# Kernel optimization log

Hardware: AMD Instinct MI355X
Metric: run time of the kernel (lower is better)

Reference implementation:

```python
import jax, jax.numpy as jnp
import numpy as np

KH = KW = 3  # fixed: distortion() generates a 9-tap (3x3) offset grid


def make_offset(h, w, dilation=1.0, skydome=True):
    """Faithful numpy port of DistortionConvLayer.distortion -> [1,h,w,9,2] (last dim = [x_off, y_off])."""
    pi = np.pi
    unit_w = 2.0 * pi / w
    unit_h = pi / (2.0 * h) if skydome else pi / h
    rho = np.tan(unit_w) * dilation
    v = np.array([0.0, 1.0, 0.0])
    r_grid = np.array([[1, -1], [1, 0], [1, 1], [0, -1], [0, 0], [0, 1], [-1, -1], [-1, 0], [-1, 1]], dtype=np.float64)
    xc = int(w * 0.5)
    theta = (xc - 0.5 * w) * unit_w
    y = np.arange(h, dtype=np.float64)
    phi = (h - y) * unit_h if skydome else (h * 0.5 - y) * unit_h  # [h]
    p_u = np.stack([np.cos(phi) * np.cos(theta), np.sin(phi), np.cos(phi) * np.sin(theta)], axis=-1)  # [h,3]
    t_x = np.cross(np.broadcast_to(v, p_u.shape), p_u)  # [h,3]
    t_y = np.cross(p_u, t_x)                            # [h,3]
    # r_sphere: [h,9,3]
    r_sphere = rho * (r_grid[None, :, 0, None] * t_x[:, None, :] + r_grid[None, :, 1, None] * t_y[:, None, :])
    p_ur = p_u[:, None, :] + r_sphere  # [h,9,3]
    ux, uy, uz = p_ur[..., 0], p_ur[..., 1], p_ur[..., 2]
    base = np.arctan2(uz, ux)
    theta_r = np.where(ux > 0, base,
               np.where(ux < 0, np.where(uz >= 0, base + pi, base - pi),
                np.where(uz > 0, pi * 0.5, -pi * 0.5)))
    phi_r = np.arcsin(uy)
    x_r = (theta_r / pi + 1.0) * 0.5 * w
    y_r = (1.0 - 2.0 * phi_r / pi) * h if skydome else (0.5 - phi_r / pi) * h
    k = np.stack([x_r, y_r], axis=-1)          # [h,9,2], entries [x, y] (as in original)
    off = k - k[:, 4:5, :]                      # subtract center tap
    off = np.broadcast_to(off[:, None, :, :], (h, w, 9, 2))  # tile over width
    return off[None].astype(np.float32)         # [1,h,w,9,2]


def setup_inputs() -> dict:
    key = jax.random.key(0)
    k1, k2 = jax.random.split(key)
    B, H, W, C, F = 4, 128, 256, 64, 128
    inputs = jax.random.normal(k1, (B, H, W, C), dtype=jnp.float32)
    fan_in = KH * KW * C
    kernel = jax.random.normal(k2, (fan_in, F), dtype=jnp.float32) * (1.0 / np.sqrt(fan_in))
    bias = jnp.zeros((F,), dtype=jnp.float32)
    return {"inputs": inputs, "kernel": kernel, "bias": bias}


def reference(inputs, kernel, bias):
    B, H, W, C = inputs.shape
    F = kernel.shape[1]
    off = jnp.asarray(make_offset(H, W))  # [1,H,W,9,2], static constant
    # 'same' padding for 3x3, stride 1, dilation 1 -> pad 1 on each side
    xp = jnp.pad(inputs, ((0, 0), (1, 1), (1, 1), (0, 0)))
    in_h, in_w = H + 2, W + 2
    # base conv sampling coordinates (extract_patches order: tap k -> dy=k//3, dx=k%3)
    dy = jnp.repeat(jnp.arange(KH), KW).astype(jnp.float32)  # [9]
    dx = jnp.tile(jnp.arange(KW), KH).astype(jnp.float32)    # [9]
    base_y = jnp.arange(H, dtype=jnp.float32)[None, :, None, None] + dy[None, None, None, :]  # [1,H,1,9]
    base_x = jnp.arange(W, dtype=jnp.float32)[None, None, :, None] + dx[None, None, None, :]  # [1,1,W,9]
    # NOTE: faithful to original: channel 0 of offset (x_r diffs) is added to y, channel 1 to x
    y = base_y + off[..., 0]  # [1,H,W,9]
    x = base_x + off[..., 1]
    y = jnp.clip(y, 0.0, in_h - 1)
    x = jnp.where(x < 0, x + in_w, x)
    x = jnp.where(x > in_w - 1, x - in_w, x)
    y0 = jnp.floor(y).astype(jnp.int32)
    x0 = jnp.floor(x).astype(jnp.int32)
    y1, x1 = y0 + 1, x0 + 1
    y0 = jnp.clip(y0, 0, in_h - 1); y1 = jnp.clip(y1, 0, in_h - 1)
    x0 = jnp.clip(x0, 0, in_w - 1); x1 = jnp.clip(x1, 0, in_w - 1)
    bidx = jnp.arange(B)[:, None, None, None]  # [B,1,1,1], broadcasts against [1,H,W,9]
    gather = lambda yi, xi: xp[bidx, yi, xi]   # -> [B,H,W,9,C]
    p0 = gather(y0, x0); p1 = gather(y0, x1); p2 = gather(y1, x0); p3 = gather(y1, x1)
    y0f, y1f = y0.astype(jnp.float32), y1.astype(jnp.float32)
    x0f, x1f = x0.astype(jnp.float32), x1.astype(jnp.float32)
    w0 = ((y1f - y) * (x1f - x))[..., None]
    w1 = ((y1f - y) * (x - x0f))[..., None]
    w2 = ((y - y0f) * (x1f - x))[..., None]
    w3 = ((y - y0f) * (x - x0f))[..., None]
    pixels = w0 * p0 + w1 * p1 + w2 * p2 + w3 * p3  # [B,H,W,9,C]
    pixels = pixels.reshape(B, H * W, KH * KW * C)
    out = pixels @ kernel + bias                    # [B,HW,F]
    return jax.nn.relu(out.reshape(B, H, W, F))
```

## Files before the change

### kernel.cpp

```cpp
#include <hip/hip_runtime.h>
#include <math.h>

#define Bb 4
#define Hh 128
#define Ww 256
#define Cc 64
#define Ff 128
#define INH 130
#define INW 258

#define WSLOT 72
#define WPW 37

typedef __attribute__((ext_vector_type(8))) __bf16 bf16x8;
typedef __attribute__((ext_vector_type(4))) float floatx4;

__device__ __forceinline__ unsigned short f2bf(float f) {
  unsigned int u = __float_as_uint(f);
  unsigned int r = u + 0x7fffu + ((u >> 16) & 1u);
  return (unsigned short)(r >> 16);
}

__device__ __forceinline__ unsigned int cvt_pk_bf16(float lo, float hi) {
  unsigned int r;
  asm("v_cvt_pk_bf16_f32 %0, %1, %2" : "=v"(r) : "v"(lo), "v"(hi));
  return r;
}

__global__ void prep_kernel(const float* __restrict__ kmat,
                            float* __restrict__ offtab,
                            unsigned short* __restrict__ kTB) {
  int gid = blockIdx.x * 256 + threadIdx.x;
  if (gid < 576 * 128) {
    int f = gid & 127;
    int k = gid >> 7;
    int tap = k >> 6;
    int r = k & 63;
    int kk = r >> 5;
    int quad = (r >> 3) & 3;
    int i = r & 7;
    int chunk = tap * 8 + kk * 4 + quad;
    kTB[((size_t)chunk * 128 + f) * 8 + i] = f2bf(kmat[gid]);
  }
  if (gid < Hh * 9) {
    int h = gid / 9;
    int j = gid - h * 9;
    const double pi = 3.14159265358979323846;
    double unit_w = 2.0 * pi / (double)Ww;
    double unit_h = pi / (2.0 * (double)Hh);
    double rho = tan(unit_w);
    double theta = ((double)(Ww / 2) - 0.5 * (double)Ww) * unit_w;
    double phi = ((double)Hh - (double)h) * unit_h;
    double cph = cos(phi), sph = sin(phi);
    double cth = cos(theta), sth = sin(theta);
    double pux = cph * cth, puy = sph, puz = cph * sth;
    double txx = puz, txy = 0.0, txz = -pux;
    double tyx = puy * txz - puz * txy;
    double tyy = puz * txx - pux * txz;
    double tyz = pux * txy - puy * txx;
    const int r0t[9] = {1, 1, 1, 0, 0, 0, -1, -1, -1};
    const int r1t[9] = {-1, 0, 1, -1, 0, 1, -1, 0, 1};
    auto proj = [&](int r0, int r1, double& xr, double& yr) {
      double ux = pux + rho * ((double)r0 * txx + (double)r1 * tyx);
      double uy = puy + rho * ((double)r0 * txy + (double)r1 * tyy);
      double uz = puz + rho * ((double)r0 * txz + (double)r1 * tyz);
      double base = atan2(uz, ux);
      double th;
      if (ux > 0.0)        th = base;
      else if (ux < 0.0)   th = (uz >= 0.0) ? base + pi : base - pi;
      else                 th = (uz > 0.0) ? pi * 0.5 : -pi * 0.5;
      double ph = asin(uy);
      xr = (th / pi + 1.0) * 0.5 * (double)Ww;
      yr = (1.0 - 2.0 * ph / pi) * (double)Hh;
    };
    double xc, yc, xj, yj;
    proj(0, 0, xc, yc);
    proj(r0t[j], r1t[j], xj, yj);
    offtab[gid * 2 + 0] = (float)(xj - xc);
    offtab[gid * 2 + 1] = (float)(yj - yc);
  }
}

__global__ __launch_bounds__(256, 3) void fused_kernel(
    const float* __restrict__ in, const float* __restrict__ bias,
    const unsigned short* __restrict__ kTB, const float* __restrict__ offtab,
    float* __restrict__ out) {
  __shared__ unsigned short winH[4 * WPW * WSLOT];

  int lidx = ((blockIdx.x & 7) << 7) | (blockIdx.x >> 3);
  int wt = lidx & 1;
  int h  = (lidx >> 1) & 127;
  int b  = lidx >> 8;
  int w0 = wt << 7;

  int tid  = threadIdx.x;
  int lane = tid & 63;
  int wave = tid >> 6;
  int m_base = wave << 5;
  int l15  = lane & 15;
  int quad = lane >> 4;

  unsigned short* win = &winH[wave * (WPW * WSLOT)];
  if (lane < 18) *(uint2*)&win[36 * WSLOT + lane * 4] = (uint2){0u, 0u};

  floatx4 acc[2][8];
#pragma unroll
  for (int i = 0; i < 2; i++)
#pragma unroll
    for (int j = 0; j < 8; j++) acc[i][j] = (floatx4){0.f, 0.f, 0.f, 0.f};

  const float* inb = in + (size_t)b * Hh * Ww * Cc;
  const bf16x8* kbase = (const bf16x8*)kTB;

  for (int tap = 0; tap < 9; tap++) {
    float off0 = offtab[(h * 9 + tap) * 2 + 0];
    float off1 = offtab[(h * 9 + tap) * 2 + 1];
    float dyk = (float)(tap / 3), dxk = (float)(tap % 3);

    float y = (float)h + dyk + off0;
    y = fminf(fmaxf(y, 0.f), (float)(INH - 1));
    int y0i = (int)floorf(y);
    int y1i = y0i + 1;
    y0i = min(max(y0i, 0), INH - 1);
    y1i = min(max(y1i, 0), INH - 1);
    float wy0 = (float)y1i - y;
    float wy1 = y - (float)y0i;
    if (!(y0i >= 1 && y0i <= Hh)) wy0 = 0.f;
    if (!(y1i >= 1 && y1i <= Hh)) wy1 = 0.f;
    const char* r0 = (const char*)(inb + (size_t)min(max(y0i - 1, 0), Hh - 1) * Ww * Cc);
    const char* r1 = (const char*)(inb + (size_t)min(max(y1i - 1, 0), Hh - 1) * Ww * Cc);

    float xrep = (float)w0 + dxk + off1;
    float flo  = floorf(xrep);
    int jb = (int)flo - 1;
    float fr = xrep - flo;
    float q00 = wy0 * (1.f - fr), q01 = wy0 * fr;
    float q10 = wy1 * (1.f - fr), q11 = wy1 * fr;

    int slotv[2];
#pragma unroll
    for (int mi = 0; mi < 2; mi++) {
      int wr = m_base + mi * 16 + l15;
      float x = (float)(w0 + wr) + dxk + off1;
      if (x < 0.f) x += (float)INW;
      if (x > (float)(INW - 1)) x -= (float)INW;
      int x0i = (int)floorf(x);
      int s = x0i - jb;
      if (s < 0) s += INW;
      int ls = s - m_base;
      if ((unsigned)ls > 35u) ls = 36;
      slotv[mi] = ls;
    }

    for (int it = 0; it < 5; it++) {
      int t = lane + (it << 6);
      if (t < 36 * 8) {
        int ls = t >> 3;
        int c8 = (t & 7) << 3;
        int col = jb + m_base + ls;
        if (col < 0) col += INW;
        if (col > INW - 1) col -= INW;
        int ncol = (col == INW - 1) ? 0 : col + 1;
        bool cok = ((unsigned)(col - 1) < (unsigned)Ww);
        bool nok = ((unsigned)(ncol - 1) < (unsigned)Ww);
        unsigned offc = (((unsigned)((col - 1) & (Ww - 1))) << 8) + ((unsigned)c8 << 2);
        unsigned offn = (((unsigned)((ncol - 1) & (Ww - 1))) << 8) + ((unsigned)c8 << 2);
        float w00 = cok ? q00 : 0.f;
        float w01 = nok ? q01 : 0.f;
        float w10 = cok ? q10 : 0.f;
        float w11 = nok ? q11 : 0.f;
        uint4 st;
        {
          float4 a0 = *(const float4*)(r0 + offc);
          float4 a1 = *(const float4*)(r0 + offn);
          float4 b0 = *(const float4*)(r1 + offc);
          float4 b1 = *(const float4*)(r1 + offn);
          float px = w00 * a0.x + w01 * a1.x + w10 * b0.x + w11 * b1.x;
          float py = w00 * a0.y + w01 * a1.y + w10 * b0.y + w11 * b1.y;
          float pz = w00 * a0.z + w01 * a1.z + w10 * b0.z + w11 * b1.z;
          float pw = w00 * a0.w + w01 * a1.w + w10 * b0.w + w11 * b1.w;
          st.x = cvt_pk_bf16(px, py);
          st.y = cvt_pk_bf16(pz, pw);
        }
        {
          float4 a0 = *(const float4*)(r0 + offc + 16);
          float4 a1 = *(const float4*)(r0 + offn + 16);
          float4 b0 = *(const float4*)(r1 + offc + 16);
          float4 b1 = *(const float4*)(r1 + offn + 16);
          float px = w00 * a0.x + w01 * a1.x + w10 * b0.x + w11 * b1.x;
          float py = w00 * a0.y + w01 * a1.y + w10 * b0.y + w11 * b1.y;
          float pz = w00 * a0.z + w01 * a1.z + w10 * b0.z + w11 * b1.z;
          float pw = w00 * a0.w + w01 * a1.w + w10 * b0.w + w11 * b1.w;
          st.z = cvt_pk_bf16(px, py);
          st.w = cvt_pk_bf16(pz, pw);
        }
        *(uint4*)(&win[ls * WSLOT + c8]) = st;
      }
    }

#pragma unroll
    for (int kk = 0; kk < 2; kk++) {
      int ch0 = (tap * 8 + kk * 4 + quad) * 128;
      bf16x8 af0 = *(const bf16x8*)&win[slotv[0] * WSLOT + kk * 32 + quad * 8];
      bf16x8 af1 = *(const bf16x8*)&win[slotv[1] * WSLOT + kk * 32 + quad * 8];
#pragma unroll
      for (int ni = 0; ni < 8; ni++) {
        bf16x8 bf = kbase[ch0 + ni * 16 + l15];
        acc[0][ni] = __builtin_amdgcn_mfma_f32_16x16x32_bf16(af0, bf, acc[0][ni], 0, 0, 0);
        acc[1][ni] = __builtin_amdgcn_mfma_f32_16x16x32_bf16(af1, bf, acc[1][ni], 0, 0, 0);
      }
    }
  }

  size_t outbase = ((size_t)(b * Hh + h) * Ww + w0);
#pragma unroll
  for (int ni = 0; ni < 8; ni++) {
    int f = ni * 16 + l15;
    float bv = bias[f];
#pragma unroll
    for (int mi = 0; mi < 2; mi++) {
#pragma unroll
      for (int r = 0; r < 4; r++) {
        int m = m_base + mi * 16 + quad * 4 + r;
        out[(outbase + m) * Ff + f] = fmaxf(acc[mi][ni][r] + bv, 0.f);
      }
    }
  }
}

extern "C" void kernel_launch(void* const* d_in, const int* in_sizes, int n_in,
                              void* d_out, int out_size, void* d_ws, size_t ws_size,
                              hipStream_t stream) {
  const float* in   = (const float*)d_in[0];
  const float* kmat = (const float*)d_in[1];
  const float* bias = (const float*)d_in[2];
  float* out = (float*)d_out;

  float* offtab = (float*)d_ws;
  unsigned short* kTB = (unsigned short*)((char*)d_ws + Hh * 9 * 2 * sizeof(float));
  if (ws_size < (size_t)(Hh * 9 * 2 * sizeof(float) + 128 * 576 * sizeof(unsigned short)))
    return;

  prep_kernel<<<288, 256, 0, stream>>>(kmat, offtab, kTB);
  fused_kernel<<<Bb * Hh * (Ww / 128), 256, 0, stream>>>(in, bias, kTB, offtab, out);
}
```

Before: 156.5 us.

## Split bilinear sampling into y-interp staging and x-interp at fragment load

The staging loop now does only the vertical interpolation, loading one column instead of two (half the global loads). It stores fp32 rows in LDS. The horizontal lerp between adjacent slots and the bf16 conversion move to the point where MFMA A fragments are read. Launch bounds go from 3 to 4 blocks per CU. This adds LDS footprint and extra LDS reads per fragment. Slot 35 now maps to the zero row, which may change edge handling slightly.

```diff
diff --git a/kernel.cpp b/kernel.cpp
--- a/kernel.cpp
+++ b/kernel.cpp
@@ -9,8 +9,8 @@
 #define INH 130
 #define INW 258
 
-#define WSLOT 72
-#define WPW 37
+#define YSTRIDE 68
+#define YSLOTS 37
 
 typedef __attribute__((ext_vector_type(8))) __bf16 bf16x8;
 typedef __attribute__((ext_vector_type(4))) float floatx4;
@@ -81,11 +81,11 @@
   }
 }
 
-__global__ __launch_bounds__(256, 3) void fused_kernel(
+__global__ __launch_bounds__(256, 4) void fused_kernel(
     const float* __restrict__ in, const float* __restrict__ bias,
     const unsigned short* __restrict__ kTB, const float* __restrict__ offtab,
     float* __restrict__ out) {
-  __shared__ unsigned short winH[4 * WPW * WSLOT];
+  __shared__ float ybH[4 * YSLOTS * YSTRIDE];
 
   int lidx = ((blockIdx.x & 7) << 7) | (blockIdx.x >> 3);
   int wt = lidx & 1;
@@ -100,8 +100,8 @@
   int l15  = lane & 15;
   int quad = lane >> 4;
 
-  unsigned short* win = &winH[wave * (WPW * WSLOT)];
-  if (lane < 18) *(uint2*)&win[36 * WSLOT + lane * 4] = (uint2){0u, 0u};
+  float* yb = &ybH[wave * (YSLOTS * YSTRIDE)];
+  if (lane < 17) *(float4*)&yb[36 * YSTRIDE + lane * 4] = (float4){0.f, 0.f, 0.f, 0.f};
 
   floatx4 acc[2][8];
 #pragma unroll
@@ -134,10 +134,9 @@
     float flo  = floorf(xrep);
     int jb = (int)flo - 1;
     float fr = xrep - flo;
-    float q00 = wy0 * (1.f - fr), q01 = wy0 * fr;
-    float q10 = wy1 * (1.f - fr), q11 = wy1 * fr;
-
-    int slotv[2];
+    float fxa = 1.f - fr, fxb = fr;
+
+    int s0v[2], s1v[2];
 #pragma unroll
     for (int mi = 0; mi < 2; mi++) {
       int wr = m_base + mi * 16 + l15;
@@ -148,66 +147,75 @@
       int s = x0i - jb;
       if (s < 0) s += INW;
       int ls = s - m_base;
-      if ((unsigned)ls > 35u) ls = 36;
-      slotv[mi] = ls;
-    }
-
+      bool ok = (unsigned)ls <= 34u;
+      s0v[mi] = ok ? ls : 36;
+      s1v[mi] = ok ? ls + 1 : 36;
+    }
+
+#pragma unroll
     for (int it = 0; it < 5; it++) {
       int t = lane + (it << 6);
-      if (t < 36 * 8) {
+      if (it < 4 || lane < 32) {
         int ls = t >> 3;
-        int c8 = (t & 7) << 3;
+        int c8f = (t & 7) << 3;
         int col = jb + m_base + ls;
         if (col < 0) col += INW;
         if (col > INW - 1) col -= INW;
-        int ncol = (col == INW - 1) ? 0 : col + 1;
         bool cok = ((unsigned)(col - 1) < (unsigned)Ww);
-        bool nok = ((unsigned)(ncol - 1) < (unsigned)Ww);
-        unsigned offc = (((unsigned)((col - 1) & (Ww - 1))) << 8) + ((unsigned)c8 << 2);
-        unsigned offn = (((unsigned)((ncol - 1) & (Ww - 1))) << 8) + ((unsigned)c8 << 2);
-        float w00 = cok ? q00 : 0.f;
-        float w01 = nok ? q01 : 0.f;
-        float w10 = cok ? q10 : 0.f;
-        float w11 = nok ? q11 : 0.f;
-        uint4 st;
-        {
-          float4 a0 = *(const float4*)(r0 + offc);
-          float4 a1 = *(const float4*)(r0 + offn);
-          float4 b0 = *(const float4*)(r1 + offc);
-          float4 b1 = *(const float4*)(r1 + offn);
-          float px = w00 * a0.x + w01 * a1.x + w10 * b0.x + w11 * b1.x;
-          float py = w00 * a0.y + w01 * a1.y + w10 * b0.y + w11 * b1.y;
-          float pz = w00 * a0.z + w01 * a1.z + w10 * b0.z + w11 * b1.z;
-          float pw = w00 * a0.w + w01 * a1.w + w10 * b0.w + w11 * b1.w;
-          st.x = cvt_pk_bf16(px, py);
-          st.y = cvt_pk_bf16(pz, pw);
-        }
-        {
-          float4 a0 = *(const float4*)(r0 + offc + 16);
-          float4 a1 = *(const float4*)(r0 + offn + 16);
-          float4 b0 = *(const float4*)(r1 + offc + 16);
-          float4 b1 = *(const float4*)(r1 + offn + 16);
-          float px = w00 * a0.x + w01 * a1.x + w10 * b0.x + w11 * b1.x;
-          float py = w00 * a0.y + w01 * a1.y + w10 * b0.y + w11 * b1.y;
-          float pz = w00 * a0.z + w01 * a1.z + w10 * b0.z + w11 * b1.z;
-          float pw = w00 * a0.w + w01 * a1.w + w10 * b0.w + w11 * b1.w;
-          st.z = cvt_pk_bf16(px, py);
-          st.w = cvt_pk_bf16(pz, pw);
-        }
-        *(uint4*)(&win[ls * WSLOT + c8]) = st;
+        unsigned offc = (((unsigned)((col - 1) & (Ww - 1))) << 8) + ((unsigned)c8f << 2);
+        float wa = cok ? wy0 : 0.f;
+        float wb = cok ? wy1 : 0.f;
+        float4 a0 = *(const float4*)(r0 + offc);
+        float4 a1 = *(const float4*)(r0 + offc + 16);
+        float4 b0 = *(const float4*)(r1 + offc);
+        float4 b1 = *(const float4*)(r1 + offc + 16);
+        float4 p0, p1;
+        p0.x = wa * a0.x + wb * b0.x;
+        p0.y = wa * a0.y + wb * b0.y;
+        p0.z = wa * a0.z + wb * b0.z;
+        p0.w = wa * a0.w + wb * b0.w;
+        p1.x = wa * a1.x + wb * b1.x;
+        p1.y = wa * a1.y + wb * b1.y;
+        p1.z = wa * a1.z + wb * b1.z;
+        p1.w = wa * a1.w + wb * b1.w;
+        float* dst = yb + ls * YSTRIDE + c8f;
+        *(float4*)dst = p0;
+        *(float4*)(dst + 4) = p1;
       }
     }
 
 #pragma unroll
     for (int kk = 0; kk < 2; kk++) {
       int ch0 = (tap * 8 + kk * 4 + quad) * 128;
-      bf16x8 af0 = *(const bf16x8*)&win[slotv[0] * WSLOT + kk * 32 + quad * 8];
-      bf16x8 af1 = *(const bf16x8*)&win[slotv[1] * WSLOT + kk * 32 + quad * 8];
+      bf16x8 af[2];
+#pragma unroll
+      for (int mi = 0; mi < 2; mi++) {
+        const float* pa = yb + s0v[mi] * YSTRIDE + kk * 32 + quad * 8;
+        const float* pb = yb + s1v[mi] * YSTRIDE + kk * 32 + quad * 8;
+        float4 ya = *(const float4*)pa;
+        float4 yA = *(const float4*)(pa + 4);
+        float4 yc = *(const float4*)pb;
+        float4 yC = *(const float4*)(pb + 4);
+        float p0 = fxa * ya.x + fxb * yc.x;
+        float p1 = fxa * ya.y + fxb * yc.y;
+        float p2 = fxa * ya.z + fxb * yc.z;
+        float p3 = fxa * ya.w + fxb * yc.w;
+        float p4 = fxa * yA.x + fxb * yC.x;
+        float p5 = fxa * yA.y + fxb * yC.y;
+        float p6 = fxa * yA.z + fxb * yC.z;
+        float p7 = fxa * yA.w + fxb * yC.w;
+        union { uint4 u; bf16x8 v; } afc;
+        afc.u.x = cvt_pk_bf16(p0, p1);
+        afc.u.y = cvt_pk_bf16(p2, p3);
+        afc.u.z = cvt_pk_bf16(p4, p5);
+        afc.u.w = cvt_pk_bf16(p6, p7);
+        af[mi] = afc.v;
+      }
 #pragma unroll
       for (int ni = 0; ni < 8; ni++) {
         bf16x8 bf = kbase[ch0 + ni * 16 + l15];
-        acc[0][ni] = __builtin_amdgcn_mfma_f32_16x16x32_bf16(af0, bf, acc[0][ni], 0, 0, 0);
-        acc[1][ni] = __builtin_amdgcn_mfma_f32_16x16x32_bf16(af1, bf, acc[1][ni], 0, 0, 0);
+        acc[0][ni] = __builtin_amdgcn_mfma_f32_16x16x32_bf16(af[0], bf, acc[0][ni], 0, 0, 0);
+        acc[1][ni] = __builtin_amdgcn_mfma_f32_16x16x32_bf16(af[1], bf, acc[1][ni], 0, 0, 0);
       }
     }
   }
```

After: 136.6 us. -12.7%, faster.
